# Performance work log

Hardware: AMD Instinct MI355X
Metric: run time of the kernel (lower is better)

Reference implementation:

```python
import jax, jax.numpy as jnp
import numpy as np

B, T, C = 4, 2048, 1024
H = 16
D = C // H  # head_dim = 64


def setup_inputs() -> dict:
    key = jax.random.key(0)
    ks = jax.random.split(key, 6)
    s = 1.0 / np.sqrt(C)
    x = jax.random.normal(ks[0], (B, T, C), dtype=jnp.float32)
    Wq = jax.random.normal(ks[1], (C, C), dtype=jnp.float32) * s
    Wk = jax.random.normal(ks[2], (C, C), dtype=jnp.float32) * s
    Wv = jax.random.normal(ks[3], (C, C), dtype=jnp.float32) * s
    Wo = jax.random.normal(ks[4], (C, C), dtype=jnp.float32) * s
    bo = jnp.zeros((C,), dtype=jnp.float32)
    # causal mask, 1 = attend, 0 = masked (masked_fill(mask==0, -inf))
    mask = jnp.broadcast_to(jnp.tril(jnp.ones((T, T), dtype=jnp.int32)), (B, T, T))
    return {"x": x, "mask": mask, "Wq": Wq, "Wk": Wk, "Wv": Wv, "Wo": Wo, "bo": bo}


def reference(x, mask, Wq, Wk, Wv, Wo, bo):
    Bx, Tx, Cx = x.shape
    # projections; nn.Linear computes x @ W.T, here W is stored as (C, C) applied as x @ W
    Q = (x @ Wq).reshape(Bx, Tx, H, D).transpose(0, 2, 1, 3)  # (B,H,T,D)
    K = (x @ Wk).reshape(Bx, Tx, H, D).transpose(0, 2, 1, 3)
    V = (x @ Wv).reshape(Bx, Tx, H, D).transpose(0, 2, 1, 3)
    scores = jnp.einsum('bhqd,bhkd->bhqk', Q, K) / jnp.sqrt(jnp.float32(D))
    scores = jnp.where(mask[:, None, :, :] == 0, -jnp.inf, scores)
    attn = jax.nn.softmax(scores, axis=-1)
    ctx = jnp.einsum('bhqk,bhkd->bhqd', attn, V)  # (B,H,T,D)
    ctx = ctx.transpose(0, 2, 1, 3).reshape(Bx, Tx, Cx)
    return ctx @ Wo + bo
```

## Files before the change

kernel.cpp:

```cpp
#include <hip/hip_runtime.h>
#include <hip/hip_bf16.h>


#define B_  4
#define T_  2048
#define C_  1024
#define H_  16
#define D_  64
#define M_  (B_*T_)

#define LOG2E 1.4426950408889634f

using bf16x8 = __attribute__((ext_vector_type(8))) short;
using f32x4  = __attribute__((ext_vector_type(4))) float;
using u16x4  = __attribute__((ext_vector_type(4))) unsigned short;

__device__ __forceinline__ unsigned short f2bf(float f) {
  union { float f; unsigned u; } cv; cv.f = f;
  unsigned u = cv.u;
  u += 0x7fffu + ((u >> 16) & 1u);
  return (unsigned short)(u >> 16);
}

__device__ __forceinline__ unsigned cvt_pk_bf16(float lo, float hi) {
  unsigned r;
  asm("v_cvt_pk_bf16_f32 %0, %1, %2" : "=v"(r) : "v"(lo), "v"(hi));
  return r;
}

__device__ __forceinline__ float exp2fast(float x) {
#if __has_builtin(__builtin_amdgcn_exp2f)
  return __builtin_amdgcn_exp2f(x);
#else
  return exp2f(x);
#endif
}

__device__ __forceinline__ void lds_load16(void* lds, const void* g) {
  __builtin_amdgcn_global_load_lds(
      (const __attribute__((address_space(1))) unsigned int*)g,
      (__attribute__((address_space(3))) unsigned int*)lds,
      16, 0, 0);
}

__global__ __launch_bounds__(256) void conv_x_kernel(
    const float* __restrict__ x, unsigned short* __restrict__ xb) {
  int i = blockIdx.x * 256 + threadIdx.x;
  const float4* xv = (const float4*)x;
  float4 a = xv[i * 2 + 0];
  float4 b = xv[i * 2 + 1];
  using u16x8 = __attribute__((ext_vector_type(8))) unsigned short;
  u16x8 o;
  o[0]=f2bf(a.x); o[1]=f2bf(a.y); o[2]=f2bf(a.z); o[3]=f2bf(a.w);
  o[4]=f2bf(b.x); o[5]=f2bf(b.y); o[6]=f2bf(b.z); o[7]=f2bf(b.w);
  *(u16x8*)&xb[(size_t)i * 8] = o;
}

__global__ __launch_bounds__(256) void conv_wt_kernel(
    const float* __restrict__ W0, const float* __restrict__ W1,
    const float* __restrict__ W2, const float* __restrict__ W3,
    unsigned short* __restrict__ WT) {
  __shared__ float tile[64][65];
  const float* W = (blockIdx.z == 0) ? W0 : (blockIdx.z == 1) ? W1
                 : (blockIdx.z == 2) ? W2 : W3;
  unsigned short* o = WT + (size_t)blockIdx.z * C_ * C_;
  const int k0 = blockIdx.y * 64, n0 = blockIdx.x * 64;
  const int tr = threadIdx.x >> 6;
  const int tc = threadIdx.x & 63;
#pragma unroll
  for (int i = 0; i < 16; ++i) {
    int k = tr + i * 4;
    tile[k][tc] = W[(size_t)(k0 + k) * C_ + n0 + tc];
  }
  __syncthreads();
#pragma unroll
  for (int i = 0; i < 16; ++i) {
    int n = tr + i * 4;
    o[(size_t)(n0 + n) * C_ + k0 + tc] = f2bf(tile[tc][n]);
  }
}

template <int EPI>
__global__ __launch_bounds__(256) void gemm128(
    const unsigned short* __restrict__ A, const unsigned short* __restrict__ BT,
    void* __restrict__ out, const float* __restrict__ bias, int K) {
  __shared__ unsigned short As[128][32];
  __shared__ unsigned short Bs[128][32];

  const int tid  = threadIdx.x;
  const int wid  = tid >> 6, lane = tid & 63;
  const int wr   = wid >> 1, wc = wid & 1;
  const int fr   = lane & 15, fq = lane >> 4;
  const int bid  = blockIdx.y * gridDim.x + blockIdx.x;
  const int xcd  = bid & 7, ii = bid >> 3;
  const int bm   = xcd + 8 * (ii & 7);
  const int bn   = ii >> 3;

  const unsigned short* aP = A  + (size_t)(bm * 128 + wid * 32 + (lane >> 2)) * K + (lane & 3) * 8;
  const unsigned short* bP = BT + (size_t)(bn * 128 + wid * 32 + (lane >> 2)) * K + (lane & 3) * 8;
  unsigned short* asB = &As[wid * 32][0];
  unsigned short* bsB = &Bs[wid * 32][0];

  f32x4 acc[4][4] = {};

  for (int k0 = 0; k0 < K; k0 += 32) {
    lds_load16(asB,           aP + k0);
    lds_load16(asB + 16 * 32, aP + (size_t)16 * K + k0);
    lds_load16(bsB,           bP + k0);
    lds_load16(bsB + 16 * 32, bP + (size_t)16 * K + k0);
    __syncthreads();

    bf16x8 af[4], bfr[4];
#pragma unroll
    for (int mi = 0; mi < 4; ++mi)
      af[mi] = *(const bf16x8*)&As[wr * 64 + mi * 16 + fr][fq * 8];
#pragma unroll
    for (int ni = 0; ni < 4; ++ni)
      bfr[ni] = *(const bf16x8*)&Bs[wc * 64 + ni * 16 + fr][fq * 8];
#pragma unroll
    for (int mi = 0; mi < 4; ++mi)
#pragma unroll
      for (int ni = 0; ni < 4; ++ni)
        acc[mi][ni] = __builtin_amdgcn_mfma_f32_16x16x32_bf16(
            af[mi], bfr[ni], acc[mi][ni], 0, 0, 0);
    __syncthreads();
  }

  if (EPI == 0) {
    unsigned short* o = (unsigned short*)out;
#pragma unroll
    for (int mi = 0; mi < 4; ++mi) {
      int m  = bm * 128 + wr * 64 + mi * 16 + fq * 4;
      int b  = m >> 11;
      int t0 = m & 2047;
#pragma unroll
      for (int ni = 0; ni < 4; ++ni) {
        int n = bn * 128 + wc * 64 + ni * 16 + fr;
        int mat = n >> 10;
        int nc  = n & 1023;
        int h = nc >> 6, d = nc & 63;
        float sc_ = (mat == 0) ? (0.125f * LOG2E) : 1.0f;
        size_t base = (size_t)mat * ((size_t)M_ * C_) + ((size_t)(b * H_ + h) << 17) + d;
#pragma unroll
        for (int r = 0; r < 4; ++r)
          o[base + (size_t)(t0 + r) * D_] = f2bf(acc[mi][ni][r] * sc_);
      }
    }
  } else {
    float* o = (float*)out;
#pragma unroll
    for (int mi = 0; mi < 4; ++mi) {
      int m = bm * 128 + wr * 64 + mi * 16 + fq * 4;
#pragma unroll
      for (int ni = 0; ni < 4; ++ni) {
        int n = bn * 128 + wc * 64 + ni * 16 + fr;
        float bv = bias[n];
#pragma unroll
        for (int r = 0; r < 4; ++r)
          o[(size_t)(m + r) * C_ + n] = acc[mi][ni][r] + bv;
      }
    }
  }
}

#define KSTR 72
__global__ __launch_bounds__(256) void attn_kernel(
    const unsigned short* __restrict__ Qg, const unsigned short* __restrict__ Kg,
    const unsigned short* __restrict__ Vg, unsigned short* __restrict__ ctx) {
  __shared__ __align__(16) unsigned short Ks[2][64][KSTR];
  __shared__ __align__(16) unsigned short VTs[2][64][KSTR];

  const int tid = threadIdx.x, wid = tid >> 6, lane = tid & 63;
  const int fr = lane & 15, fq = lane >> 4;

  const int bid = blockIdx.x;
  const int xcd = bid & 7, j = bid >> 3;
  const int bh = xcd * 8 + (j & 7);
  const int qt = 15 - (j >> 3);
  const int b = bh >> 4, h = bh & 15;
  const size_t base = (size_t)bh * (T_ * D_);

  const int ksr = tid >> 2, ksc = tid & 3;
  const int kpr = ((ksr >> 5) & 1) * 32 + ((ksr >> 2) & 1) * 16 +
                  ((ksr >> 3) & 3) * 4 + (ksr & 3);
  const unsigned short* Kptr = Kg + base + (size_t)ksr * D_ + ksc * 8;
  const int vc = tid >> 5, vr_ = tid & 31;
  const unsigned short* Vptr = Vg + base + (size_t)(2 * vr_) * D_ + vc * 8;

  int4 kr0, kr1, va, vb;
  auto stage_load = [&](int kv) {
    const unsigned short* kp = Kptr + (size_t)kv * D_;
    kr0 = *(const int4*)kp;
    kr1 = *(const int4*)(kp + 32);
    const unsigned short* vp = Vptr + (size_t)kv * D_;
    va = *(const int4*)vp;
    vb = *(const int4*)(vp + D_);
  };
  auto stage_write = [&](int nb) {
    *(int4*)&Ks[nb][kpr][ksc * 8]       = kr0;
    *(int4*)&Ks[nb][kpr][(ksc + 4) * 8] = kr1;
    const unsigned short* pa = (const unsigned short*)&va;
    const unsigned short* pb = (const unsigned short*)&vb;
#pragma unroll
    for (int i = 0; i < 8; ++i) {
      unsigned w = (unsigned)pa[i] | ((unsigned)pb[i] << 16);
      *(unsigned*)&VTs[nb][vc * 8 + i][2 * vr_] = w;
    }
  };

  stage_load(0);
  stage_write(0);

  const int qbase = qt * 128;

  bf16x8 qf[2][2];
#pragma unroll
  for (int x = 0; x < 2; ++x)
#pragma unroll
    for (int t = 0; t < 2; ++t)
      qf[x][t] = *(const bf16x8*)
          &Qg[base + (size_t)(qbase + 64 * x + wid * 16 + fr) * D_ + t * 32 + fq * 8];

  f32x4 acc[2][4] = {};
  float m_run[2] = {-__builtin_inff(), -__builtin_inff()};
  float l_run[2] = {0.f, 0.f};

  const int nsteps = 2 * qt + 2;
  int kv0 = 0;
  for (int s = 0; s < nsteps; ++s) {
    const int  cur = s & 1;
    const bool have_next = (s + 1 < nsteps);

    __syncthreads();
    if (have_next) stage_load(kv0 + 64);

    bf16x8 kf[8];
#pragma unroll
    for (int nt = 0; nt < 4; ++nt)
#pragma unroll
      for (int t = 0; t < 2; ++t)
        kf[nt * 2 + t] = *(const bf16x8*)&Ks[cur][nt * 16 + fr][t * 32 + fq * 8];

    bf16x8 pf[2][2];
#pragma unroll
    for (int x = 0; x < 2; ++x) {
      f32x4 sv[4];
      __builtin_amdgcn_s_setprio(1);
#pragma unroll
      for (int nt = 0; nt < 4; ++nt) {
        f32x4 sa = {};
        sa = __builtin_amdgcn_mfma_f32_16x16x32_bf16(kf[nt * 2 + 0], qf[x][0], sa, 0, 0, 0);
        sa = __builtin_amdgcn_mfma_f32_16x16x32_bf16(kf[nt * 2 + 1], qf[x][1], sa, 0, 0, 0);
        sv[nt] = sa;
      }
      __builtin_amdgcn_s_setprio(0);

      float mt = -__builtin_inff();
      if (kv0 >= qbase + 64 * x) {
        const int qi = qbase + 64 * x + wid * 16 + fr;
#pragma unroll
        for (int nt = 0; nt < 4; ++nt)
#pragma unroll
          for (int r = 0; r < 4; ++r) {
            int kvi = kv0 + 32 * (nt >> 1) + 8 * fq + 4 * (nt & 1) + r;
            float v = sv[nt][r];
            if (kvi > qi) v = -__builtin_inff();
            sv[nt][r] = v;
            mt = fmaxf(mt, v);
          }
      } else {
#pragma unroll
        for (int nt = 0; nt < 4; ++nt)
          mt = fmaxf(mt, fmaxf(fmaxf(sv[nt][0], sv[nt][1]),
                               fmaxf(sv[nt][2], sv[nt][3])));
      }
      mt = fmaxf(mt, __shfl_xor(mt, 16));
      mt = fmaxf(mt, __shfl_xor(mt, 32));

      if (__any(mt > m_run[x] + 8.0f)) {
        float mn = fmaxf(m_run[x], mt);
        float c  = exp2fast(m_run[x] - mn);
        m_run[x] = mn;
#pragma unroll
        for (int dt = 0; dt < 4; ++dt) acc[x][dt] *= c;
        l_run[x] *= c;
      }

      float lsum = 0.f;
      int pw[8];
#pragma unroll
      for (int nt = 0; nt < 4; ++nt) {
        float p0 = exp2fast(sv[nt][0] - m_run[x]);
        float p1 = exp2fast(sv[nt][1] - m_run[x]);
        float p2 = exp2fast(sv[nt][2] - m_run[x]);
        float p3 = exp2fast(sv[nt][3] - m_run[x]);
        lsum += (p0 + p1) + (p2 + p3);
        pw[(nt >> 1) * 4 + (nt & 1) * 2 + 0] = (int)cvt_pk_bf16(p0, p1);
        pw[(nt >> 1) * 4 + (nt & 1) * 2 + 1] = (int)cvt_pk_bf16(p2, p3);
      }
      lsum += __shfl_xor(lsum, 16);
      lsum += __shfl_xor(lsum, 32);
      l_run[x] += lsum;

#pragma unroll
      for (int t = 0; t < 2; ++t) {
        int4 v4 = {pw[t * 4 + 0], pw[t * 4 + 1], pw[t * 4 + 2], pw[t * 4 + 3]};
        pf[x][t] = __builtin_bit_cast(bf16x8, v4);
      }
    }

    __builtin_amdgcn_s_setprio(1);
#pragma unroll
    for (int t = 0; t < 2; ++t)
#pragma unroll
      for (int dt = 0; dt < 4; ++dt) {
        bf16x8 vf = *(const bf16x8*)&VTs[cur][dt * 16 + fr][t * 32 + fq * 8];
        acc[0][dt] = __builtin_amdgcn_mfma_f32_16x16x32_bf16(vf, pf[0][t], acc[0][dt], 0, 0, 0);
        acc[1][dt] = __builtin_amdgcn_mfma_f32_16x16x32_bf16(vf, pf[1][t], acc[1][dt], 0, 0, 0);
      }
    __builtin_amdgcn_s_setprio(0);

    if (have_next) stage_write(cur ^ 1);
    kv0 += 64;
  }

#pragma unroll
  for (int x = 0; x < 2; ++x) {
    float linv = 1.0f / l_run[x];
    unsigned short* orow =
        ctx + (size_t)(b * T_ + qbase + 64 * x + wid * 16 + fr) * C_ + h * D_;
#pragma unroll
    for (int dt = 0; dt < 4; ++dt) {
      u16x4 o;
#pragma unroll
      for (int r = 0; r < 4; ++r) o[r] = f2bf(acc[x][dt][r] * linv);
      *(u16x4*)&orow[dt * 16 + fq * 4] = o;
    }
  }
}

extern "C" void kernel_launch(void* const* d_in, const int* in_sizes, int n_in,
                              void* d_out, int out_size, void* d_ws, size_t ws_size,
                              hipStream_t stream) {
  const float* x  = (const float*)d_in[0];
  const float* Wq = (const float*)d_in[2];
  const float* Wk = (const float*)d_in[3];
  const float* Wv = (const float*)d_in[4];
  const float* Wo = (const float*)d_in[5];
  const float* bo = (const float*)d_in[6];

  unsigned short* xb  = (unsigned short*)d_ws;
  unsigned short* wqt = xb  + (size_t)M_ * C_;
  unsigned short* wot = wqt + (size_t)3 * C_ * C_;
  unsigned short* Qb  = wot + (size_t)C_ * C_;
  unsigned short* ctxb = xb;

  conv_x_kernel<<<4096, 256, 0, stream>>>(x, xb);
  conv_wt_kernel<<<dim3(16, 16, 4), 256, 0, stream>>>(Wq, Wk, Wv, Wo, wqt);

  gemm128<0><<<dim3(24, M_ / 128), 256, 0, stream>>>(xb, wqt, Qb, nullptr, C_);

  attn_kernel<<<dim3(1024), 256, 0, stream>>>(
      Qb, Qb + (size_t)M_ * C_, Qb + (size_t)2 * M_ * C_, ctxb);

  gemm128<1><<<dim3(8, M_ / 128), 256, 0, stream>>>(ctxb, wot, d_out, bo, C_);
}
```

Baseline: 191.1 us.

## Use 128-wide KV tiles with single-buffered LDS in attention kernel

The attention kernel now processes 128 keys per step instead of 64, which halves the loop trip count and the barrier count. It drops LDS double buffering in favor of a single buffer guarded by two barriers, and requests 3 blocks per CU via launch bounds. The row-sum reduction across lanes is deferred to the epilogue, and P·V is done per query half right after its softmax. Risks include added register pressure from holding 16 score vectors and 8 prefetch registers, an extra barrier per step, and wasted causal work on the larger diagonal tile.

```diff
diff --git a/kernel.cpp b/kernel.cpp
--- a/kernel.cpp
+++ b/kernel.cpp
@@ -163,12 +163,13 @@
   }
 }
 
-#define KSTR 72
-__global__ __launch_bounds__(256) void attn_kernel(
+#define KSK 72
+#define KSV 136
+__global__ __launch_bounds__(256, 3) void attn_kernel(
     const unsigned short* __restrict__ Qg, const unsigned short* __restrict__ Kg,
     const unsigned short* __restrict__ Vg, unsigned short* __restrict__ ctx) {
-  __shared__ __align__(16) unsigned short Ks[2][64][KSTR];
-  __shared__ __align__(16) unsigned short VTs[2][64][KSTR];
+  __shared__ __align__(16) unsigned short Ks[128][KSK];
+  __shared__ __align__(16) unsigned short VTs[64][KSV];
 
   const int tid = threadIdx.x, wid = tid >> 6, lane = tid & 63;
   const int fr = lane & 15, fq = lane >> 4;
@@ -180,36 +181,41 @@
   const int b = bh >> 4, h = bh & 15;
   const size_t base = (size_t)bh * (T_ * D_);
 
-  const int ksr = tid >> 2, ksc = tid & 3;
-  const int kpr = ((ksr >> 5) & 1) * 32 + ((ksr >> 2) & 1) * 16 +
-                  ((ksr >> 3) & 3) * 4 + (ksr & 3);
-  const unsigned short* Kptr = Kg + base + (size_t)ksr * D_ + ksc * 8;
+  const int ksr = tid >> 1, khalf = tid & 1;
+  const int kpr = (ksr & 96) | ((ksr >> 2) & 1) * 16 |
+                  ((ksr >> 3) & 3) * 4 | (ksr & 3);
+  const unsigned short* Kptr = Kg + base + (size_t)ksr * D_ + khalf * 32;
   const int vc = tid >> 5, vr_ = tid & 31;
-  const unsigned short* Vptr = Vg + base + (size_t)(2 * vr_) * D_ + vc * 8;
-
-  int4 kr0, kr1, va, vb;
+  const unsigned short* Vptr = Vg + base + (size_t)(4 * vr_) * D_ + vc * 8;
+
+  int4 kr[4], vv[4];
   auto stage_load = [&](int kv) {
     const unsigned short* kp = Kptr + (size_t)kv * D_;
-    kr0 = *(const int4*)kp;
-    kr1 = *(const int4*)(kp + 32);
+#pragma unroll
+    for (int jj = 0; jj < 4; ++jj) kr[jj] = *(const int4*)(kp + 8 * jj);
     const unsigned short* vp = Vptr + (size_t)kv * D_;
-    va = *(const int4*)vp;
-    vb = *(const int4*)(vp + D_);
+#pragma unroll
+    for (int k = 0; k < 4; ++k) vv[k] = *(const int4*)(vp + (size_t)k * D_);
   };
-  auto stage_write = [&](int nb) {
-    *(int4*)&Ks[nb][kpr][ksc * 8]       = kr0;
-    *(int4*)&Ks[nb][kpr][(ksc + 4) * 8] = kr1;
-    const unsigned short* pa = (const unsigned short*)&va;
-    const unsigned short* pb = (const unsigned short*)&vb;
+  auto stage_write = [&]() {
+#pragma unroll
+    for (int jj = 0; jj < 4; ++jj)
+      *(int4*)&Ks[kpr][khalf * 32 + 8 * jj] = kr[jj];
+    const unsigned short* p0 = (const unsigned short*)&vv[0];
+    const unsigned short* p1 = (const unsigned short*)&vv[1];
+    const unsigned short* p2 = (const unsigned short*)&vv[2];
+    const unsigned short* p3 = (const unsigned short*)&vv[3];
 #pragma unroll
     for (int i = 0; i < 8; ++i) {
-      unsigned w = (unsigned)pa[i] | ((unsigned)pb[i] << 16);
-      *(unsigned*)&VTs[nb][vc * 8 + i][2 * vr_] = w;
+      uint2 w;
+      w.x = (unsigned)p0[i] | ((unsigned)p1[i] << 16);
+      w.y = (unsigned)p2[i] | ((unsigned)p3[i] << 16);
+      *(uint2*)&VTs[vc * 8 + i][4 * vr_] = w;
     }
   };
 
   stage_load(0);
-  stage_write(0);
+  stage_write();
 
   const int qbase = qt * 128;
 
@@ -225,41 +231,35 @@
   float m_run[2] = {-__builtin_inff(), -__builtin_inff()};
   float l_run[2] = {0.f, 0.f};
 
-  const int nsteps = 2 * qt + 2;
+  const int nsteps = qt + 1;
   int kv0 = 0;
   for (int s = 0; s < nsteps; ++s) {
-    const int  cur = s & 1;
     const bool have_next = (s + 1 < nsteps);
+    const bool diag = (kv0 == qbase);
 
     __syncthreads();
-    if (have_next) stage_load(kv0 + 64);
-
-    bf16x8 kf[8];
-#pragma unroll
-    for (int nt = 0; nt < 4; ++nt)
-#pragma unroll
-      for (int t = 0; t < 2; ++t)
-        kf[nt * 2 + t] = *(const bf16x8*)&Ks[cur][nt * 16 + fr][t * 32 + fq * 8];
-
-    bf16x8 pf[2][2];
+    if (have_next) stage_load(kv0 + 128);
+
 #pragma unroll
     for (int x = 0; x < 2; ++x) {
-      f32x4 sv[4];
+      f32x4 sv[8];
       __builtin_amdgcn_s_setprio(1);
 #pragma unroll
-      for (int nt = 0; nt < 4; ++nt) {
+      for (int nt = 0; nt < 8; ++nt) {
+        bf16x8 kf0 = *(const bf16x8*)&Ks[nt * 16 + fr][fq * 8];
+        bf16x8 kf1 = *(const bf16x8*)&Ks[nt * 16 + fr][32 + fq * 8];
         f32x4 sa = {};
-        sa = __builtin_amdgcn_mfma_f32_16x16x32_bf16(kf[nt * 2 + 0], qf[x][0], sa, 0, 0, 0);
-        sa = __builtin_amdgcn_mfma_f32_16x16x32_bf16(kf[nt * 2 + 1], qf[x][1], sa, 0, 0, 0);
+        sa = __builtin_amdgcn_mfma_f32_16x16x32_bf16(kf0, qf[x][0], sa, 0, 0, 0);
+        sa = __builtin_amdgcn_mfma_f32_16x16x32_bf16(kf1, qf[x][1], sa, 0, 0, 0);
         sv[nt] = sa;
       }
       __builtin_amdgcn_s_setprio(0);
 
       float mt = -__builtin_inff();
-      if (kv0 >= qbase + 64 * x) {
+      if (diag) {
         const int qi = qbase + 64 * x + wid * 16 + fr;
 #pragma unroll
-        for (int nt = 0; nt < 4; ++nt)
+        for (int nt = 0; nt < 8; ++nt)
 #pragma unroll
           for (int r = 0; r < 4; ++r) {
             int kvi = kv0 + 32 * (nt >> 1) + 8 * fq + 4 * (nt & 1) + r;
@@ -270,7 +270,7 @@
           }
       } else {
 #pragma unroll
-        for (int nt = 0; nt < 4; ++nt)
+        for (int nt = 0; nt < 8; ++nt)
           mt = fmaxf(mt, fmaxf(fmaxf(sv[nt][0], sv[nt][1]),
                                fmaxf(sv[nt][2], sv[nt][3])));
       }
@@ -286,47 +286,44 @@
         l_run[x] *= c;
       }
 
-      float lsum = 0.f;
-      int pw[8];
-#pragma unroll
-      for (int nt = 0; nt < 4; ++nt) {
+      int pw[16];
+#pragma unroll
+      for (int nt = 0; nt < 8; ++nt) {
         float p0 = exp2fast(sv[nt][0] - m_run[x]);
         float p1 = exp2fast(sv[nt][1] - m_run[x]);
         float p2 = exp2fast(sv[nt][2] - m_run[x]);
         float p3 = exp2fast(sv[nt][3] - m_run[x]);
-        lsum += (p0 + p1) + (p2 + p3);
+        l_run[x] += (p0 + p1) + (p2 + p3);
         pw[(nt >> 1) * 4 + (nt & 1) * 2 + 0] = (int)cvt_pk_bf16(p0, p1);
         pw[(nt >> 1) * 4 + (nt & 1) * 2 + 1] = (int)cvt_pk_bf16(p2, p3);
       }
-      lsum += __shfl_xor(lsum, 16);
-      lsum += __shfl_xor(lsum, 32);
-      l_run[x] += lsum;
-
-#pragma unroll
-      for (int t = 0; t < 2; ++t) {
+
+      __builtin_amdgcn_s_setprio(1);
+#pragma unroll
+      for (int t = 0; t < 4; ++t) {
         int4 v4 = {pw[t * 4 + 0], pw[t * 4 + 1], pw[t * 4 + 2], pw[t * 4 + 3]};
-        pf[x][t] = __builtin_bit_cast(bf16x8, v4);
-      }
-    }
-
-    __builtin_amdgcn_s_setprio(1);
-#pragma unroll
-    for (int t = 0; t < 2; ++t)
-#pragma unroll
-      for (int dt = 0; dt < 4; ++dt) {
-        bf16x8 vf = *(const bf16x8*)&VTs[cur][dt * 16 + fr][t * 32 + fq * 8];
-        acc[0][dt] = __builtin_amdgcn_mfma_f32_16x16x32_bf16(vf, pf[0][t], acc[0][dt], 0, 0, 0);
-        acc[1][dt] = __builtin_amdgcn_mfma_f32_16x16x32_bf16(vf, pf[1][t], acc[1][dt], 0, 0, 0);
-      }
-    __builtin_amdgcn_s_setprio(0);
-
-    if (have_next) stage_write(cur ^ 1);
-    kv0 += 64;
+        bf16x8 pft = __builtin_bit_cast(bf16x8, v4);
+#pragma unroll
+        for (int dt = 0; dt < 4; ++dt) {
+          bf16x8 vf = *(const bf16x8*)&VTs[dt * 16 + fr][t * 32 + fq * 8];
+          acc[x][dt] = __builtin_amdgcn_mfma_f32_16x16x32_bf16(vf, pft, acc[x][dt], 0, 0, 0);
+        }
+      }
+      __builtin_amdgcn_s_setprio(0);
+    }
+
+    __syncthreads();
+    if (have_next) stage_write();
+
+    kv0 += 128;
   }
 
 #pragma unroll
   for (int x = 0; x < 2; ++x) {
-    float linv = 1.0f / l_run[x];
+    float l = l_run[x];
+    l += __shfl_xor(l, 16);
+    l += __shfl_xor(l, 32);
+    float linv = 1.0f / l;
     unsigned short* orow =
         ctx + (size_t)(b * T_ + qbase + 64 * x + wid * 16 + fr) * C_ + h * D_;
 #pragma unroll
```

After: 237.9 us. 24.5% more time.
